# Optimization experiments

Hardware: AMD Instinct MI355X
Metric: run time of the kernel (lower is better)

Reference implementation:

```python
import jax, jax.numpy as jnp
import numpy as np

B, S, DD, DE, DA = 32, 2048, 1024, 1024, 1024
NEG = -1000000000.0


def setup_inputs() -> dict:
    key = jax.random.key(0)
    k1, k2, k3, k4, k5 = jax.random.split(key, 5)
    query_state = jax.random.normal(k1, (B, DD), dtype=jnp.float32)
    encoder_hidden_states = jax.random.normal(k2, (B, S, DE), dtype=jnp.float32)
    attention_mask = jax.random.randint(k3, (B, S), 0, 2, dtype=jnp.int32)
    # W_c: Linear(DD+DE -> DA, bias=False): weight shape [DA, DD+DE]
    W_c = jax.random.normal(k4, (DA, DD + DE), dtype=jnp.float32) / np.sqrt(DD + DE)
    # V: Linear(DA -> 1, bias=False): weight shape [1, DA]
    V = jax.random.normal(k5, (1, DA), dtype=jnp.float32) / np.sqrt(DA)
    return {
        "query_state": query_state,
        "encoder_hidden_states": encoder_hidden_states,
        "attention_mask": attention_mask,
        "W_c": W_c,
        "V": V,
    }


def reference(query_state, encoder_hidden_states, attention_mask, W_c, V):
    # Split W_c along input dim: cat([q, e]) @ W_c.T == q @ Wq.T + e @ We.T
    Wq = W_c[:, :DD]          # [DA, DD]
    We = W_c[:, DD:]          # [DA, DE]
    q_proj = jnp.einsum('bd,ad->ba', query_state, Wq)            # [B, DA]
    e_proj = jnp.einsum('bsd,ad->bsa', encoder_hidden_states, We)  # [B, S, DA]
    energies = jnp.tanh(q_proj[:, None, :] + e_proj)             # [B, S, DA]
    scores = jnp.einsum('bsa,a->bs', energies, V[0])             # [B, S]
    scores = jnp.where(attention_mask == 0, NEG, scores)
    attention_weights = jax.nn.softmax(scores, axis=1)           # [B, S]
    context_vector = jnp.einsum('bs,bsd->bd', attention_weights, encoder_hidden_states)
    return context_vector, attention_weights
```

## Files before the change

kernel.cpp:

```cpp
#include <hip/hip_runtime.h>
#include <hip/hip_bf16.h>

#define NB 32
#define NS 2048
#define NDD 1024
#define NDE 1024
#define NDA 1024
#define NEGV (-1000000000.0f)

typedef __attribute__((ext_vector_type(8))) __bf16 bf16x8;
typedef __attribute__((ext_vector_type(4))) float f32x4;

__device__ __forceinline__ float fast_tanh(float x) {
    x = fminf(10.0f, fmaxf(-10.0f, x));
    float e = __expf(2.0f * x);
    return __fdividef(e - 1.0f, e + 1.0f);
}

__global__ void prep_we(const float* __restrict__ Wc, __bf16* __restrict__ We) {
    int f = blockIdx.x * 256 + threadIdx.x;
    int a  = f >> 8;
    int k4 = f & 255;
    float4 v = *reinterpret_cast<const float4*>(Wc + (size_t)a * (NDD + NDE) + NDD + k4 * 4);
    union { __bf16 h[4]; uint2 u; } pk;
    pk.h[0] = (__bf16)v.x; pk.h[1] = (__bf16)v.y;
    pk.h[2] = (__bf16)v.z; pk.h[3] = (__bf16)v.w;
    *reinterpret_cast<uint2*>(We + (size_t)a * NDE + k4 * 4) = pk.u;
}

__global__ void qproj_kernel(const float* __restrict__ q, const float* __restrict__ Wc,
                             float* __restrict__ qp) {
    __shared__ float qs[NDD];
    int b = blockIdx.y;
    int a = blockIdx.x * 256 + threadIdx.x;
    float4 qv = *reinterpret_cast<const float4*>(q + (size_t)b * NDD + threadIdx.x * 4);
    *reinterpret_cast<float4*>(qs + threadIdx.x * 4) = qv;
    __syncthreads();
    const float* wrow = Wc + (size_t)a * (NDD + NDE);
    float acc = 0.f;
#pragma unroll 4
    for (int k4 = 0; k4 < 256; ++k4) {
        float4 w = *reinterpret_cast<const float4*>(wrow + k4 * 4);
        acc += qs[k4*4+0] * w.x + qs[k4*4+1] * w.y + qs[k4*4+2] * w.z + qs[k4*4+3] * w.w;
    }
    qp[(size_t)b * NDA + a] = acc;
}

__global__ __launch_bounds__(256, 4) void score_kernel(
    const float* __restrict__ E, const __bf16* __restrict__ We,
    const float* __restrict__ qp, const float* __restrict__ Vv,
    float* __restrict__ scores_p) {
    __shared__ __align__(16) __bf16 As[2][128 * 32];
    __shared__ __align__(16) __bf16 Bs[2][128 * 32];
    __shared__ float ps_lds[128][2];

    const int tid    = threadIdx.x;
    const int lane   = tid & 63;
    const int lane15 = lane & 15;
    const int h      = lane >> 4;
    const int wid    = tid >> 6;
    const int wr     = wid >> 1;
    const int wc     = wid & 1;

    const int bid = blockIdx.x;
    const int xcd = bid & 7;
    const int j   = bid >> 3;
    const int m   = xcd * 64 + (j >> 3);
    const int n   = j & 7;
    const int row0  = m * 128;
    const int ncol0 = n * 128;
    const int b     = m >> 4;

    f32x4 acc[4][4];
#pragma unroll
    for (int mi = 0; mi < 4; ++mi)
#pragma unroll
        for (int ni = 0; ni < 4; ++ni)
            acc[mi][ni] = (f32x4){0.f, 0.f, 0.f, 0.f};

    const int wbyte = wid * 1024;

    float4 st[4];

#define A_LOAD(kc)                                                                     \
    {                                                                                  \
        _Pragma("unroll")                                                              \
        for (int i = 0; i < 4; ++i)                                                    \
            st[i] = *reinterpret_cast<const float4*>(                                  \
                E + (size_t)(row0 + i * 32 + (tid >> 3)) * NDE + (kc) + (tid & 7) * 4);\
    }

#define A_WRITE(buf)                                                                   \
    {                                                                                  \
        _Pragma("unroll")                                                              \
        for (int i = 0; i < 4; ++i) {                                                  \
            int r  = i * 32 + (tid >> 3);                                              \
            int sl = ((tid & 7) >> 1) ^ ((r >> 1) & 3);                                \
            union { __bf16 hh[4]; uint2 u; } pk;                                       \
            pk.hh[0] = (__bf16)st[i].x; pk.hh[1] = (__bf16)st[i].y;                    \
            pk.hh[2] = (__bf16)st[i].z; pk.hh[3] = (__bf16)st[i].w;                    \
            *reinterpret_cast<uint2*>((char*)&As[buf][0] + r * 64 + sl * 16 + (tid & 1) * 8) = pk.u; \
        }                                                                              \
    }

#define B_STAGE(buf, kc)                                                               \
    {                                                                                  \
        _Pragma("unroll")                                                              \
        for (int i = 0; i < 2; ++i) {                                                  \
            int ib = i * 4096 + tid * 16;                                              \
            int r  = ib >> 6;                                                          \
            int sl = (ib >> 4) & 3;                                                    \
            int sg = sl ^ ((r >> 1) & 3);                                              \
            const __bf16* g = We + (size_t)(ncol0 + r) * NDE + (kc) + sg * 8;          \
            __builtin_amdgcn_global_load_lds(                                          \
                (const __attribute__((address_space(1))) unsigned*)g,                  \
                (__attribute__((address_space(3))) unsigned*)((char*)&Bs[buf][0] + i * 4096 + wbyte), \
                16, 0, 0);                                                             \
        }                                                                              \
    }

    A_LOAD(0)
    B_STAGE(0, 0)
    A_WRITE(0)
    __syncthreads();

    for (int it = 0; it < 32; ++it) {
        const int cur = it & 1;
        if (it < 31) {
            A_LOAD((it + 1) * 32)
            B_STAGE(cur ^ 1, (it + 1) * 32)
        }
        const char* Ab = (const char*)&As[cur][0];
        const char* Bb = (const char*)&Bs[cur][0];
        bf16x8 bfr[4], afr[4];
#pragma unroll
        for (int ni = 0; ni < 4; ++ni) {
            int cr = wc * 64 + ni * 16 + lane15;
            bfr[ni] = *reinterpret_cast<const bf16x8*>(Bb + cr * 64 + ((h ^ ((cr >> 1) & 3)) * 16));
        }
#pragma unroll
        for (int mi = 0; mi < 4; ++mi) {
            int r = wr * 64 + mi * 16 + lane15;
            afr[mi] = *reinterpret_cast<const bf16x8*>(Ab + r * 64 + ((h ^ ((r >> 1) & 3)) * 16));
        }
#pragma unroll
        for (int mi = 0; mi < 4; ++mi)
#pragma unroll
            for (int ni = 0; ni < 4; ++ni)
                acc[mi][ni] = __builtin_amdgcn_mfma_f32_16x16x32_bf16(afr[mi], bfr[ni], acc[mi][ni], 0, 0, 0);
        if (it < 31) A_WRITE(cur ^ 1)
        __syncthreads();
    }

    float qv[4], vv[4];
#pragma unroll
    for (int ni = 0; ni < 4; ++ni) {
        int col = ncol0 + wc * 64 + ni * 16 + lane15;
        qv[ni] = qp[(size_t)b * NDA + col];
        vv[ni] = Vv[col];
    }
#pragma unroll
    for (int mi = 0; mi < 4; ++mi)
#pragma unroll
        for (int jj = 0; jj < 4; ++jj) {
            float s = 0.f;
#pragma unroll
            for (int ni = 0; ni < 4; ++ni)
                s += fast_tanh(qv[ni] + acc[mi][ni][jj]) * vv[ni];
            s += __shfl_xor(s, 1);
            s += __shfl_xor(s, 2);
            s += __shfl_xor(s, 4);
            s += __shfl_xor(s, 8);
            if (lane15 == 0)
                ps_lds[wr * 64 + mi * 16 + h * 4 + jj][wc] = s;
        }
    __syncthreads();
    if (tid < 128)
        scores_p[(size_t)n * (NB * NS) + row0 + tid] = ps_lds[tid][0] + ps_lds[tid][1];
}

__global__ void softmax_kernel(const float* __restrict__ sp, const int* __restrict__ mask,
                               float* __restrict__ wout) {
    int b = blockIdx.x;
    const int* mrow = mask + (size_t)b * NS;
    float v[8];
    float lmax = -INFINITY;
#pragma unroll
    for (int jj = 0; jj < 8; ++jj) {
        int s = threadIdx.x + 256 * jj;
        float sc = 0.f;
#pragma unroll
        for (int nn = 0; nn < 8; ++nn) sc += sp[(size_t)nn * (NB * NS) + b * NS + s];
        v[jj] = (mrow[s] == 0) ? NEGV : sc;
        lmax = fmaxf(lmax, v[jj]);
    }
#pragma unroll
    for (int mm = 1; mm <= 32; mm <<= 1) lmax = fmaxf(lmax, __shfl_xor(lmax, mm));
    __shared__ float redm[4], reds[4];
    if ((threadIdx.x & 63) == 0) redm[threadIdx.x >> 6] = lmax;
    __syncthreads();
    float bmax = fmaxf(fmaxf(redm[0], redm[1]), fmaxf(redm[2], redm[3]));
    float lsum = 0.f;
#pragma unroll
    for (int jj = 0; jj < 8; ++jj) { v[jj] = __expf(v[jj] - bmax); lsum += v[jj]; }
#pragma unroll
    for (int mm = 1; mm <= 32; mm <<= 1) lsum += __shfl_xor(lsum, mm);
    if ((threadIdx.x & 63) == 0) reds[threadIdx.x >> 6] = lsum;
    __syncthreads();
    float inv = __fdividef(1.0f, reds[0] + reds[1] + reds[2] + reds[3]);
#pragma unroll
    for (int jj = 0; jj < 8; ++jj) wout[(size_t)b * NS + threadIdx.x + 256 * jj] = v[jj] * inv;
}

__global__ void context_kernel(const float* __restrict__ E, const float* __restrict__ w,
                               float* __restrict__ ctx) {
    int b  = blockIdx.x >> 3;
    int dc = blockIdx.x & 7;
    int d2 = dc * 64 + (threadIdx.x & 63);
    int s0 = (threadIdx.x >> 6) * 512;
    const float2* Eb = reinterpret_cast<const float2*>(E) + (size_t)b * NS * (NDE / 2);
    const float* wb = w + (size_t)b * NS;
    float ax = 0.f, ay = 0.f;
#pragma unroll 8
    for (int s = s0; s < s0 + 512; ++s) {
        float ws = wb[s];
        float2 e = Eb[(size_t)s * (NDE / 2) + d2];
        ax = fmaf(ws, e.x, ax);
        ay = fmaf(ws, e.y, ay);
    }
    __shared__ float2 part[256];
    part[threadIdx.x] = make_float2(ax, ay);
    __syncthreads();
    if (threadIdx.x < 64) {
        float2 p0 = part[threadIdx.x], p1 = part[threadIdx.x + 64];
        float2 p2 = part[threadIdx.x + 128], p3 = part[threadIdx.x + 192];
        float2 r = make_float2(p0.x + p1.x + p2.x + p3.x, p0.y + p1.y + p2.y + p3.y);
        reinterpret_cast<float2*>(ctx + (size_t)b * NDD + dc * 128)[threadIdx.x] = r;
    }
}

extern "C" void kernel_launch(void* const* d_in, const int* in_sizes, int n_in,
                              void* d_out, int out_size, void* d_ws, size_t ws_size,
                              hipStream_t stream) {
    const float* query = (const float*)d_in[0];
    const float* enc   = (const float*)d_in[1];
    const int*   mask  = (const int*)d_in[2];
    const float* Wc    = (const float*)d_in[3];
    const float* V     = (const float*)d_in[4];

    float* out = (float*)d_out;
    float* ctx = out;
    float* wts = out + NB * NDD;

    char* ws = (char*)d_ws;
    __bf16* We     = (__bf16*)ws;
    float*  qp     = (float*)(ws + (size_t)NDA * NDE * 2);
    float*  sp     = (float*)(ws + (size_t)NDA * NDE * 2 + NB * NDA * 4);

    hipLaunchKernelGGL(prep_we,        dim3(1024),  dim3(256), 0, stream, Wc, We);
    hipLaunchKernelGGL(qproj_kernel,   dim3(4, NB), dim3(256), 0, stream, query, Wc, qp);
    hipLaunchKernelGGL(score_kernel,   dim3(4096),  dim3(256), 0, stream, enc, We, qp, V, sp);
    hipLaunchKernelGGL(softmax_kernel, dim3(NB),    dim3(256), 0, stream, sp, mask, wts);
    hipLaunchKernelGGL(context_kernel, dim3(256),   dim3(256), 0, stream, enc, wts, ctx);
}
```

Baseline: 358.9 us.

## Pre-convert encoder states to bf16 and stream tiles via global_load_lds

Adds a prep kernel that converts the whole fp32 encoder tensor to bf16 in the workspace. A new score kernel then stages bf16 tiles straight into LDS with global_load_lds, which removes per-tile register conversion and halves the bytes read in the GEMM loop. The cost is an extra full pass over the 256MB encoder tensor plus a 128MB write, and a large workspace requirement. The original fp32 kernel is kept as a fallback when the workspace is too small.

```diff
diff --git a/kernel.cpp b/kernel.cpp
--- a/kernel.cpp
+++ b/kernel.cpp
@@ -28,6 +28,16 @@
     *reinterpret_cast<uint2*>(We + (size_t)a * NDE + k4 * 4) = pk.u;
 }
 
+__global__ void prep_e(const float* __restrict__ E, __bf16* __restrict__ Eb) {
+    size_t i = ((size_t)blockIdx.x * 256 + threadIdx.x) * 8;
+    float4 x = *reinterpret_cast<const float4*>(E + i);
+    float4 y = *reinterpret_cast<const float4*>(E + i + 4);
+    union { __bf16 h[8]; uint4 u; } pk;
+    pk.h[0] = (__bf16)x.x; pk.h[1] = (__bf16)x.y; pk.h[2] = (__bf16)x.z; pk.h[3] = (__bf16)x.w;
+    pk.h[4] = (__bf16)y.x; pk.h[5] = (__bf16)y.y; pk.h[6] = (__bf16)y.z; pk.h[7] = (__bf16)y.w;
+    *reinterpret_cast<uint4*>(Eb + i) = pk.u;
+}
+
 __global__ void qproj_kernel(const float* __restrict__ q, const float* __restrict__ Wc,
                              float* __restrict__ qp) {
     __shared__ float qs[NDD];
@@ -46,8 +56,8 @@
     qp[(size_t)b * NDA + a] = acc;
 }
 
-__global__ __launch_bounds__(256, 4) void score_kernel(
-    const float* __restrict__ E, const __bf16* __restrict__ We,
+__global__ __launch_bounds__(256) void score_kernel_bf16(
+    const __bf16* __restrict__ Eb, const __bf16* __restrict__ We,
     const float* __restrict__ qp, const float* __restrict__ Vv,
     float* __restrict__ scores_p) {
     __shared__ __align__(16) __bf16 As[2][128 * 32];
@@ -80,6 +90,113 @@
 
     const int wbyte = wid * 1024;
 
+#define STG(SRC, base_row, LDSBUF, kc)                                                 \
+    {                                                                                  \
+        _Pragma("unroll")                                                              \
+        for (int i = 0; i < 2; ++i) {                                                  \
+            int ib = i * 4096 + tid * 16;                                              \
+            int r  = ib >> 6;                                                          \
+            int sl = (ib >> 4) & 3;                                                    \
+            int sg = sl ^ ((r >> 1) & 3);                                              \
+            const __bf16* g = SRC + (size_t)((base_row) + r) * 1024 + (kc) + sg * 8;   \
+            __builtin_amdgcn_global_load_lds(                                          \
+                (const __attribute__((address_space(1))) unsigned*)g,                  \
+                (__attribute__((address_space(3))) unsigned*)((char*)LDSBUF + i * 4096 + wbyte), \
+                16, 0, 0);                                                             \
+        }                                                                              \
+    }
+
+    STG(Eb, row0, &As[0][0], 0)
+    STG(We, ncol0, &Bs[0][0], 0)
+    __syncthreads();
+
+    for (int it = 0; it < 32; ++it) {
+        const int cur = it & 1;
+        if (it < 31) {
+            STG(Eb, row0, &As[cur ^ 1][0], (it + 1) * 32)
+            STG(We, ncol0, &Bs[cur ^ 1][0], (it + 1) * 32)
+        }
+        const char* Ab = (const char*)&As[cur][0];
+        const char* Bb = (const char*)&Bs[cur][0];
+        bf16x8 bfr[4], afr[4];
+#pragma unroll
+        for (int ni = 0; ni < 4; ++ni) {
+            int cr = wc * 64 + ni * 16 + lane15;
+            bfr[ni] = *reinterpret_cast<const bf16x8*>(Bb + cr * 64 + ((h ^ ((cr >> 1) & 3)) * 16));
+        }
+#pragma unroll
+        for (int mi = 0; mi < 4; ++mi) {
+            int r = wr * 64 + mi * 16 + lane15;
+            afr[mi] = *reinterpret_cast<const bf16x8*>(Ab + r * 64 + ((h ^ ((r >> 1) & 3)) * 16));
+        }
+#pragma unroll
+        for (int mi = 0; mi < 4; ++mi)
+#pragma unroll
+            for (int ni = 0; ni < 4; ++ni)
+                acc[mi][ni] = __builtin_amdgcn_mfma_f32_16x16x32_bf16(afr[mi], bfr[ni], acc[mi][ni], 0, 0, 0);
+        __syncthreads();
+    }
+
+    float qv[4], vv[4];
+#pragma unroll
+    for (int ni = 0; ni < 4; ++ni) {
+        int col = ncol0 + wc * 64 + ni * 16 + lane15;
+        qv[ni] = qp[(size_t)b * NDA + col];
+        vv[ni] = Vv[col];
+    }
+#pragma unroll
+    for (int mi = 0; mi < 4; ++mi)
+#pragma unroll
+        for (int jj = 0; jj < 4; ++jj) {
+            float s = 0.f;
+#pragma unroll
+            for (int ni = 0; ni < 4; ++ni)
+                s += fast_tanh(qv[ni] + acc[mi][ni][jj]) * vv[ni];
+            s += __shfl_xor(s, 1);
+            s += __shfl_xor(s, 2);
+            s += __shfl_xor(s, 4);
+            s += __shfl_xor(s, 8);
+            if (lane15 == 0)
+                ps_lds[wr * 64 + mi * 16 + h * 4 + jj][wc] = s;
+        }
+    __syncthreads();
+    if (tid < 128)
+        scores_p[(size_t)n * (NB * NS) + row0 + tid] = ps_lds[tid][0] + ps_lds[tid][1];
+}
+
+__global__ __launch_bounds__(256, 4) void score_kernel_f32(
+    const float* __restrict__ E, const __bf16* __restrict__ We,
+    const float* __restrict__ qp, const float* __restrict__ Vv,
+    float* __restrict__ scores_p) {
+    __shared__ __align__(16) __bf16 As[2][128 * 32];
+    __shared__ __align__(16) __bf16 Bs[2][128 * 32];
+    __shared__ float ps_lds[128][2];
+
+    const int tid    = threadIdx.x;
+    const int lane   = tid & 63;
+    const int lane15 = lane & 15;
+    const int h      = lane >> 4;
+    const int wid    = tid >> 6;
+    const int wr     = wid >> 1;
+    const int wc     = wid & 1;
+
+    const int bid = blockIdx.x;
+    const int xcd = bid & 7;
+    const int j   = bid >> 3;
+    const int m   = xcd * 64 + (j >> 3);
+    const int n   = j & 7;
+    const int row0  = m * 128;
+    const int ncol0 = n * 128;
+    const int b     = m >> 4;
+
+    f32x4 acc[4][4];
+#pragma unroll
+    for (int mi = 0; mi < 4; ++mi)
+#pragma unroll
+        for (int ni = 0; ni < 4; ++ni)
+            acc[mi][ni] = (f32x4){0.f, 0.f, 0.f, 0.f};
+
+    const int wbyte = wid * 1024;
     float4 st[4];
 
 #define A_LOAD(kc)                                                                     \
@@ -252,14 +369,26 @@
     float* ctx = out;
     float* wts = out + NB * NDD;
 
+    const size_t WE_B = (size_t)NDA * NDE * 2;
+    const size_t QP_B = (size_t)NB * NDA * 4;
+    const size_t SP_B = (size_t)8 * NB * NS * 4;
+    const size_t EB_B = (size_t)NB * NS * NDE * 2;
+
     char* ws = (char*)d_ws;
-    __bf16* We     = (__bf16*)ws;
-    float*  qp     = (float*)(ws + (size_t)NDA * NDE * 2);
-    float*  sp     = (float*)(ws + (size_t)NDA * NDE * 2 + NB * NDA * 4);
-
-    hipLaunchKernelGGL(prep_we,        dim3(1024),  dim3(256), 0, stream, Wc, We);
-    hipLaunchKernelGGL(qproj_kernel,   dim3(4, NB), dim3(256), 0, stream, query, Wc, qp);
-    hipLaunchKernelGGL(score_kernel,   dim3(4096),  dim3(256), 0, stream, enc, We, qp, V, sp);
-    hipLaunchKernelGGL(softmax_kernel, dim3(NB),    dim3(256), 0, stream, sp, mask, wts);
-    hipLaunchKernelGGL(context_kernel, dim3(256),   dim3(256), 0, stream, enc, wts, ctx);
-}
+    __bf16* We = (__bf16*)ws;
+    float*  qp = (float*)(ws + WE_B);
+    float*  sp = (float*)(ws + WE_B + QP_B);
+    __bf16* Eb = (__bf16*)(ws + WE_B + QP_B + SP_B);
+
+    hipLaunchKernelGGL(prep_we,      dim3(1024),  dim3(256), 0, stream, Wc, We);
+    hipLaunchKernelGGL(qproj_kernel, dim3(4, NB), dim3(256), 0, stream, query, Wc, qp);
+
+    if (ws_size >= WE_B + QP_B + SP_B + EB_B) {
+        hipLaunchKernelGGL(prep_e,           dim3(32768), dim3(256), 0, stream, enc, Eb);
+        hipLaunchKernelGGL(score_kernel_bf16,dim3(4096),  dim3(256), 0, stream, Eb, We, qp, V, sp);
+    } else {
+        hipLaunchKernelGGL(score_kernel_f32, dim3(4096),  dim3(256), 0, stream, enc, We, qp, V, sp);
+    }
+    hipLaunchKernelGGL(softmax_kernel, dim3(NB),  dim3(256), 0, stream, sp, mask, wts);
+    hipLaunchKernelGGL(context_kernel, dim3(256), dim3(256), 0, stream, enc, wts, ctx);
+}
```

After: 390.8 us. 8.9% more time.
